# Kernel tuning notes

Measured on AMD Instinct MI355X. Metric: run time of the kernel, lower is better.

Reference implementation:

```python
import jax, jax.numpy as jnp
import numpy as np

N_OPS = 8  # eset_ops_3_to_3: identity, 3 single-axis sums, 3 pair sums, full sum (broadcast back)


def _conv(x, w, b):
    # x: (N,C,H,W), w: (O,C,kh,kw), VALID conv, stride 1
    y = jax.lax.conv_general_dilated(x, w, (1, 1), 'VALID',
                                     dimension_numbers=('NCHW', 'OIHW', 'NCHW'))
    return y + b[None, :, None, None]


def _maxpool2(x):
    return jax.lax.reduce_window(x, -jnp.inf, jax.lax.max,
                                 (1, 1, 2, 2), (1, 1, 2, 2), 'VALID')


def _eq3to3(x, W, b):
    # x: (B,i,j,k,d) channels-last; W: (N_OPS,d,o); b: (o,)
    # Fused form: contract each summed basis op with its weight BEFORE broadcasting.
    si = x.sum(1)          # (B,j,k,d)
    sj = x.sum(2)          # (B,i,k,d)
    sk = x.sum(3)          # (B,i,j,d)
    sij = x.sum((1, 2))    # (B,k,d)
    sik = x.sum((1, 3))    # (B,j,d)
    sjk = x.sum((2, 3))    # (B,i,d)
    s = x.sum((1, 2, 3))   # (B,d)
    y = jnp.einsum('bijkd,do->bijko', x, W[0])
    y = y + jnp.einsum('bjkd,do->bjko', si, W[1])[:, None]
    y = y + jnp.einsum('bikd,do->biko', sj, W[2])[:, :, None]
    y = y + jnp.einsum('bijd,do->bijo', sk, W[3])[:, :, :, None]
    y = y + jnp.einsum('bkd,do->bko', sij, W[4])[:, None, None]
    y = y + jnp.einsum('bjd,do->bjo', sik, W[5])[:, None, :, None]
    y = y + jnp.einsum('bid,do->bio', sjk, W[6])[:, :, None, None]
    y = y + jnp.einsum('bd,do->bo', s, W[7])[:, None, None, None]
    return y + b


def setup_inputs() -> dict:
    key = jax.random.key(0)
    ks = jax.random.split(key, 14)
    B, k, h, w = 16, 40, 28, 28
    hid, out_dim = 64, 32
    flat = 64 * 4 * 4  # after conv5-pool2-conv5-pool2 on 28x28
    p = lambda ki, shape, fan: jax.random.normal(ki, shape, jnp.float32) / np.sqrt(fan)
    return {
        'x': jax.random.normal(ks[0], (B, k, h, w), jnp.float32),
        'conv1_w': p(ks[1], (32, 1, 5, 5), 25),
        'conv1_b': jnp.zeros((32,), jnp.float32),
        'conv2_w': p(ks[2], (64, 32, 5, 5), 32 * 25),
        'conv2_b': jnp.zeros((64,), jnp.float32),
        'fc_w': p(ks[3], (flat, hid), flat),
        'fc_b': jnp.zeros((hid,), jnp.float32),
        'eq1_w': p(ks[4], (N_OPS, hid, hid), N_OPS * hid) * 0.1,
        'eq1_b': jnp.zeros((hid,), jnp.float32),
        'eq2_w': p(ks[5], (N_OPS, hid, out_dim), N_OPS * hid) * 0.1,
        'eq2_b': jnp.zeros((out_dim,), jnp.float32),
        'out_w': p(ks[6], (out_dim, 1), out_dim),
        'out_b': jnp.zeros((1,), jnp.float32),
    }


def reference(x, conv1_w, conv1_b, conv2_w, conv2_b, fc_w, fc_b,
              eq1_w, eq1_b, eq2_w, eq2_b, out_w, out_b):
    B, k, h, w = x.shape
    z = x.reshape(B * k, 1, h, w)
    z = _maxpool2(jax.nn.relu(_conv(z, conv1_w, conv1_b)))
    z = _maxpool2(jax.nn.relu(_conv(z, conv2_w, conv2_b)))
    z = z.reshape(B * k, -1) @ fc_w + fc_b
    e = jax.nn.relu(z).reshape(B, k, -1)          # (B,k,d)
    t = jnp.einsum('bid,bjd,bkd->bijkd', e, e, e)  # (B,k,k,k,d) cubic tensor
    y = jax.nn.relu(_eq3to3(t, eq1_w, eq1_b))
    y = _eq3to3(y, eq2_w, eq2_b)                   # (B,k,k,k,out_dim)
    y = jax.nn.relu(y).sum(axis=(1, 2, 3))         # (B,out_dim); dropout_prob=0 (eval)
    y = jax.nn.relu(y)
    return y @ out_w + out_b                       # (B,1)
```

## Files before the change

kernel.cpp:

```cpp
#include <hip/hip_runtime.h>
#include <hip/hip_bf16.h>


typedef unsigned short u16;
typedef __attribute__((ext_vector_type(8))) short bf8_t;
typedef __attribute__((ext_vector_type(4))) float f4_t;

#define LSTR 72

__device__ inline u16 f2bf(float f){
  union { float f; unsigned u; } v; v.f = f;
  unsigned r = v.u + 0x7fffu + ((v.u >> 16) & 1u);
  return (u16)(r >> 16);
}
__device__ inline float bflo(unsigned u){ union { unsigned x; float f; } v; v.x = u << 16; return v.f; }
__device__ inline float bfhi(unsigned u){ union { unsigned x; float f; } v; v.x = u & 0xffff0000u; return v.f; }
__device__ inline unsigned pack2(float a, float b){ return (unsigned)f2bf(a) | ((unsigned)f2bf(b) << 16); }
__device__ inline unsigned cvtpk(float lo, float hi){
  __hip_bfloat162 h2 = __float22bfloat162_rn(make_float2(lo, hi));
  union { __hip_bfloat162 h; unsigned u; } c; c.h = h2; return c.u;
}
__device__ inline void unpack8(bf8_t x, float* o){
  union { bf8_t v; unsigned u[4]; } q; q.v = x;
  #pragma unroll
  for (int p = 0; p < 4; ++p){ o[2*p] = bflo(q.u[p]); o[2*p+1] = bfhi(q.u[p]); }
}

__global__ __launch_bounds__(256) void kconv1(const float* __restrict__ x, const float* __restrict__ w1,
                                              const float* __restrict__ b1, u16* __restrict__ z1t,
                                              const float* __restrict__ w2, const float* __restrict__ fcw,
                                              u16* __restrict__ wt2, u16* __restrict__ fcwT){
  __shared__ float simg[784];
  int img = blockIdx.x, tid = threadIdx.x;
  if (img >= 640){
    int t = (img - 640)*256 + tid, stride = 32*256;
    for (int i = t; i < 51200; i += stride){
      int tap = i >> 11, rc = i & 2047, co = rc >> 5, ci = rc & 31;
      wt2[i] = f2bf(w2[co*800 + ci*25 + tap]);
    }
    for (int i = t; i < 65536; i += stride){
      int o = i >> 10, k = i & 1023;
      fcwT[i] = f2bf(fcw[k*64 + o]);
    }
    return;
  }
  for (int i = tid; i < 784; i += 256) simg[i] = x[img*784 + i];
  const int c = tid & 31;
  float wc[25];
  #pragma unroll
  for (int t = 0; t < 25; ++t) wc[t] = w1[c*25 + t];
  const float bb = b1[c];
  __syncthreads();
  #pragma unroll 2
  for (int it = 0; it < 18; ++it){
    int p = (tid >> 5) + it*8;
    int py = p / 12, px = p % 12;
    float patch[36];
    const float* sp = &simg[2*py*28 + 2*px];
    #pragma unroll
    for (int yy = 0; yy < 6; ++yy)
      #pragma unroll
      for (int xx = 0; xx < 6; ++xx) patch[yy*6+xx] = sp[yy*28+xx];
    float mx = -1e30f;
    #pragma unroll
    for (int sy = 0; sy < 2; ++sy)
    #pragma unroll
    for (int sx = 0; sx < 2; ++sx){
      float s = bb;
      #pragma unroll
      for (int dy = 0; dy < 5; ++dy)
        #pragma unroll
        for (int dx = 0; dx < 5; ++dx)
          s += patch[(sy+dy)*6 + sx+dx] * wc[dy*5+dx];
      mx = fmaxf(mx, s);
    }
    z1t[(size_t)img*4608 + p*32 + c] = f2bf(fmaxf(mx, 0.f));
  }
}

__global__ __launch_bounds__(256) void kconv2m(const u16* __restrict__ z1t, const u16* __restrict__ wt2,
                                               const float* __restrict__ b2, u16* __restrict__ z2g){
  __shared__ __align__(16) u16 sz[4608];
  __shared__ __align__(16) u16 sz2[1024];
  int img = blockIdx.x, tid = threadIdx.x;
  for (int i = tid; i < 576; i += 256)
    ((uint4*)sz)[i] = ((const uint4*)(z1t + (size_t)img*4608))[i];
  __syncthreads();
  const int wave = tid >> 6, lane = tid & 63, l15 = lane & 15, quad = lane >> 4;
  const int y = wave*2 + (l15 >> 3), x = l15 & 7;
  f4_t acc[4];
  acc[0] = (f4_t){0.f,0.f,0.f,0.f}; acc[1] = acc[0]; acc[2] = acc[0]; acc[3] = acc[0];
  #pragma unroll
  for (int dy = 0; dy < 5; ++dy)
    #pragma unroll
    for (int dx = 0; dx < 5; ++dx){
      const int tap = dy*5 + dx;
      bf8_t af = *(const bf8_t*)&sz[((y+dy)*12 + (x+dx))*32 + quad*8];
      const u16* wp = wt2 + tap*2048 + l15*32 + quad*8;
      #pragma unroll
      for (int nt = 0; nt < 4; ++nt){
        bf8_t bf = *(const bf8_t*)(wp + nt*512);
        acc[nt] = __builtin_amdgcn_mfma_f32_16x16x32_bf16(af, bf, acc[nt], 0, 0, 0);
      }
    }
  #pragma unroll
  for (int nt = 0; nt < 4; ++nt){
    int co = nt*16 + l15;
    float v0 = fmaxf(acc[nt][0], acc[nt][1]);
    float v1 = fmaxf(acc[nt][2], acc[nt][3]);
    v0 = fmaxf(v0, __shfl_xor(v0, 32));
    v1 = fmaxf(v1, __shfl_xor(v1, 32));
    if (quad < 2){
      float bb = b2[co];
      sz2[co*16 + wave*4 + quad*2 + 0] = f2bf(fmaxf(v0 + bb, 0.f));
      sz2[co*16 + wave*4 + quad*2 + 1] = f2bf(fmaxf(v1 + bb, 0.f));
    }
  }
  __syncthreads();
  if (tid < 128) ((uint4*)(z2g + (size_t)img*1024))[tid] = ((const uint4*)sz2)[tid];
}

__global__ __launch_bounds__(256) void kfc(const u16* __restrict__ z2g, const u16* __restrict__ fcwT,
                                           const float* __restrict__ fcb,
                                           float* __restrict__ e_f, u16* __restrict__ e_b){
  __shared__ __align__(16) u16 sA[16*1032];
  int img0 = blockIdx.x*16, tid = threadIdx.x;
  for (int i = tid; i < 2048; i += 256){
    int row = i >> 7, c16 = i & 127;
    ((uint4*)(sA + row*1032))[c16] = ((const uint4*)(z2g + (size_t)(img0+row)*1024))[c16];
  }
  __syncthreads();
  const int wave = tid >> 6, lane = tid & 63, l15 = lane & 15, quad = lane >> 4;
  const int o = wave*16 + l15;
  f4_t acc = (f4_t){0.f,0.f,0.f,0.f};
  #pragma unroll 8
  for (int ks = 0; ks < 32; ++ks){
    bf8_t af = *(const bf8_t*)&sA[l15*1032 + ks*32 + quad*8];
    bf8_t bf = *(const bf8_t*)(fcwT + (size_t)o*1024 + ks*32 + quad*8);
    acc = __builtin_amdgcn_mfma_f32_16x16x32_bf16(af, bf, acc, 0, 0, 0);
  }
  const float bb = fcb[o];
  #pragma unroll
  for (int r = 0; r < 4; ++r){
    int img = img0 + quad*4 + r;
    float v = fmaxf(acc[r] + bb, 0.f);
    e_f[img*64 + o] = v;
    e_b[img*64 + o] = f2bf(v);
  }
}

__global__ __launch_bounds__(256) void kprep(const float* __restrict__ e_f, const float* __restrict__ e1w,
    const float* __restrict__ e1b, const float* __restrict__ e2w,
    float* __restrict__ Sg, u16* __restrict__ Vt, float* __restrict__ c0,
    float* __restrict__ P5, float* __restrict__ P6, u16* __restrict__ W2T0,
    u16* __restrict__ W3St){
  int b = blockIdx.x, ph = blockIdx.y, tid = threadIdx.x;
  __shared__ float se[2560];
  __shared__ float S[64], S2[64], S3[64];
  for (int i = tid; i < 2560; i += 256) se[i] = e_f[b*2560 + i];
  __syncthreads();
  if (tid < 64){
    float s = 0.f;
    for (int i = 0; i < 40; ++i) s += se[i*64 + tid];
    S[tid] = s; S2[tid] = s*s; S3[tid] = s*s*s;
    if (ph == 0) Sg[b*64 + tid] = s;
  }
  __syncthreads();
  {
    const int m = ph;
    for (int idx = tid; idx < 4096; idx += 256){
      int o = idx >> 6, d = idx & 63;
      float v;
      if (m == 0)      v = e1w[d*64 + o];
      else if (m == 1) v = S[d] * e1w[4096  + d*64 + o];
      else if (m == 2) v = S[d] * e1w[8192  + d*64 + o];
      else             v = S2[d] * e1w[16384 + d*64 + o];
      Vt[(size_t)b*16384 + m*4096 + idx] = f2bf(v);
    }
  }
  if (ph == 0){
    if (tid < 64){
      float a = e1b[tid];
      for (int d = 0; d < 64; ++d) a += S3[d] * e1w[7*4096 + d*64 + tid];
      c0[b*64 + tid] = a;
    }
  } else if (ph == 1){
    for (int idx = tid; idx < 4096; idx += 256){
      int o = idx >> 6, d = idx & 63;
      W3St[(size_t)b*4096 + idx] = f2bf(S[d] * e1w[3*4096 + d*64 + o]);
    }
  } else {
    int lo = (ph == 2) ? 0 : 1280, hi = lo + 1280;
    for (int idx = lo + tid; idx < hi; idx += 256){
      int j = idx >> 6, o = idx & 63;
      float a5 = 0.f, a6 = 0.f;
      for (int d = 0; d < 64; ++d){
        float es = se[j*64 + d] * S2[d];
        a5 += es * e1w[5*4096 + d*64 + o];
        a6 += es * e1w[6*4096 + d*64 + o];
      }
      P5[(b*40+j)*64 + o] = a5;
      P6[(b*40+j)*64 + o] = a6;
    }
    if (ph == 3 && b == 0){
      for (int idx = tid; idx < 2048; idx += 256){
        int o = idx >> 6, d = idx & 63;
        W2T0[o*64 + d] = f2bf(e2w[d*32 + o]);
      }
    }
  }
}

__global__ __launch_bounds__(256) void kpq(const u16* __restrict__ e_b, const u16* __restrict__ W3St,
    const float* __restrict__ P5, const float* __restrict__ P6, const float* __restrict__ c0,
    float* __restrict__ Q3c){
  __shared__ __align__(16) u16 sP[48*LSTR];
  __shared__ __align__(16) u16 sW[64*LSTR];
  int blk = blockIdx.x, b = blk/40, i = blk%40, tid = threadIdx.x;
  const int wave = tid >> 6, lane = tid & 63, l15 = lane & 15, quad = lane >> 4;
  for (int idx = tid; idx < 2048; idx += 256){
    int o = idx >> 5, c = idx & 31;
    ((unsigned*)(sW + o*LSTR))[c] = ((const unsigned*)(W3St + (size_t)b*4096))[idx];
  }
  const unsigned* eb32 = (const unsigned*)(e_b + (size_t)b*2560);
  const unsigned* el = eb32 + i*32;
  #pragma unroll
  for (int it = 0; it < 6; ++it){
    int idx = tid + it*256;
    int k = idx >> 5, d2 = idx & 31;
    unsigned pv = 0;
    if (k < 40){
      unsigned ul = el[d2], uk = eb32[k*32 + d2];
      pv = pack2(bflo(ul)*bflo(uk), bfhi(ul)*bfhi(uk));
    }
    ((unsigned*)(sP + k*LSTR))[d2] = pv;
  }
  __syncthreads();
  bf8_t wf[2];
  #pragma unroll
  for (int ks = 0; ks < 2; ++ks)
    wf[ks] = *(const bf8_t*)&sW[(wave*16 + l15)*LSTR + ks*32 + quad*8];
  f4_t acc[3];
  #pragma unroll
  for (int n = 0; n < 3; ++n){
    f4_t a = (f4_t){0.f,0.f,0.f,0.f};
    #pragma unroll
    for (int ks = 0; ks < 2; ++ks){
      bf8_t pkf = *(const bf8_t*)&sP[(n*16 + l15)*LSTR + ks*32 + quad*8];
      a = __builtin_amdgcn_mfma_f32_16x16x32_bf16(wf[ks], pkf, a, 0, 0, 0);
    }
    acc[n] = a;
  }
  const int obase = wave*16 + quad*4;
  f4_t p6v = *(const f4_t*)&P6[(b*40+i)*64 + obase];
  f4_t c0v = *(const f4_t*)&c0[b*64 + obase];
  #pragma unroll
  for (int n = 0; n < 3; ++n){
    int j = n*16 + l15;
    if (j < 40){
      f4_t p5v = *(const f4_t*)&P5[(b*40+j)*64 + obase];
      f4_t outv = acc[n] + p5v + p6v + c0v;
      *(f4_t*)&Q3c[((size_t)((b*40+i)*40 + j))*64 + obase] = outv;
    }
  }
}

__global__ __launch_bounds__(256, 4) void kh01(
    const u16* __restrict__ e_b, const float* __restrict__ e_f,
    const u16* __restrict__ Vt, const float* __restrict__ Q3c,
    float* __restrict__ si2, float* __restrict__ sj2, float* __restrict__ sk2)
{
  __shared__ __align__(16) char smem[25344];
  u16*   sU  = (u16*)smem;
  u16*   sB1 = (u16*)(smem + 6912);
  u16*   sB0 = (u16*)(smem + 16128);
  float* sUf = (float*)smem;
  const int tid = threadIdx.x;
  const int b = blockIdx.x / 40, fix = blockIdx.x % 40;
  const int mode = blockIdx.y;
  const int wave = tid >> 6, lane = tid & 63, l15 = lane & 15, quad = lane >> 4;
  const f4_t z4 = (f4_t){0.f,0.f,0.f,0.f};

  for (int idx = tid; idx < 1536; idx += 256){
    int r = idx >> 5, c = idx & 31;
    unsigned v = (r < 40) ? ((const unsigned*)e_b)[(b*40 + r)*32 + c] : 0u;
    ((unsigned*)(sU + r*LSTR))[c] = v;
  }
  float efr[10];
  #pragma unroll
  for (int t = 0; t < 10; ++t) efr[t] = e_f[b*2560 + tid + t*256];
  const unsigned* eg = (const unsigned*)(e_b + (size_t)(b*40 + fix)*64);
  const unsigned* Vb = (const unsigned*)(Vt + (size_t)b*16384);
  for (int idx = tid; idx < 2048; idx += 256){
    int o = idx >> 5, d2 = idx & 31;
    unsigned eu = eg[d2];
    unsigned v0 = Vb[o*32 + d2];
    unsigned vA = Vb[(2-mode)*2048 + o*32 + d2];
    unsigned vB = Vb[(1+mode)*2048 + o*32 + d2];
    unsigned v3 = Vb[3*2048 + o*32 + d2];
    float e0 = bflo(eu), e1 = bfhi(eu);
    ((unsigned*)(sB1 + o*LSTR))[d2] = pack2(e0*bflo(v0)+bflo(vA), e1*bfhi(v0)+bfhi(vA));
    ((unsigned*)(sB0 + o*LSTR))[d2] = pack2(e0*bflo(vB)+bflo(v3), e1*bfhi(vB)+bfhi(v3));
  }
  __syncthreads();

  f4_t b1v[4];
  bf8_t ua[3][2];
  f4_t Y0[3];
  {
    bf8_t b0f[2], b1f[2];
    float tmp[8];
    #pragma unroll
    for (int ks = 0; ks < 2; ++ks){
      b1f[ks] = *(const bf8_t*)&sB1[(wave*16 + l15)*LSTR + ks*32 + quad*8];
      b0f[ks] = *(const bf8_t*)&sB0[(wave*16 + l15)*LSTR + ks*32 + quad*8];
      unpack8(b1f[ks], tmp);
      b1v[2*ks]   = (f4_t){tmp[0],tmp[1],tmp[2],tmp[3]};
      b1v[2*ks+1] = (f4_t){tmp[4],tmp[5],tmp[6],tmp[7]};
    }
    #pragma unroll
    for (int n = 0; n < 3; ++n){
      f4_t a = z4;
      #pragma unroll
      for (int ks = 0; ks < 2; ++ks){
        ua[n][ks] = *(const bf8_t*)&sU[(n*16 + l15)*LSTR + ks*32 + quad*8];
        a = __builtin_amdgcn_mfma_f32_16x16x32_bf16(b0f[ks], ua[n][ks], a, 0, 0, 0);
      }
      Y0[n] = a;
    }
  }
  __syncthreads();
  #pragma unroll
  for (int t = 0; t < 10; ++t) sUf[tid + t*256] = efr[t];
  __syncthreads();

  const int obase = wave*16 + quad*4;
  const float km = (l15 < 8) ? 1.f : 0.f;
  const f4_t km4 = (f4_t){km, km, km, km};
  f4_t sacc[3];
  sacc[0] = z4; sacc[1] = z4; sacc[2] = z4;

  auto qaddr = [&](int l) -> const f4_t* {
    int qidx = mode ? (fix*40 + l) : (l*40 + fix);
    return (const f4_t*)&Q3c[((size_t)(b*1600 + qidx))*64 + obase];
  };
  f4_t cadd_n = *qaddr(0);
  for (int l = 0; l < 40; ++l){
    f4_t cadd = cadd_n;
    if (l < 39) cadd_n = *qaddr(l + 1);
    const float* ep = &sUf[l*64 + quad*8];
    f4_t p00 = b1v[0] * *(const f4_t*)(ep);
    f4_t p01 = b1v[1] * *(const f4_t*)(ep + 4);
    f4_t p10 = b1v[2] * *(const f4_t*)(ep + 32);
    f4_t p11 = b1v[3] * *(const f4_t*)(ep + 36);
    union { bf8_t v; unsigned u[4]; } m0, m1;
    m0.u[0] = cvtpk(p00[0], p00[1]); m0.u[1] = cvtpk(p00[2], p00[3]);
    m0.u[2] = cvtpk(p01[0], p01[1]); m0.u[3] = cvtpk(p01[2], p01[3]);
    m1.u[0] = cvtpk(p10[0], p10[1]); m1.u[1] = cvtpk(p10[2], p10[3]);
    m1.u[2] = cvtpk(p11[0], p11[1]); m1.u[3] = cvtpk(p11[2], p11[3]);
    f4_t khs = z4;
    #pragma unroll
    for (int n = 0; n < 3; ++n){
      f4_t a = Y0[n];
      a = __builtin_amdgcn_mfma_f32_16x16x32_bf16(m0.v, ua[n][0], a, 0, 0, 0);
      a = __builtin_amdgcn_mfma_f32_16x16x32_bf16(m1.v, ua[n][1], a, 0, 0, 0);
      f4_t h = __builtin_elementwise_max(a + cadd, z4);
      sacc[n] += h;
      if (mode == 0) khs += (n == 2) ? h * km4 : h;
    }
    if (mode == 0){
      #pragma unroll
      for (int r = 0; r < 4; ++r){
        float v = khs[r];
        v += __shfl_xor(v, 1); v += __shfl_xor(v, 2);
        v += __shfl_xor(v, 4); v += __shfl_xor(v, 8);
        khs[r] = v;
      }
      if (l15 == 0)
        *(f4_t*)&sk2[((size_t)((b*40 + l)*40 + fix))*64 + obase] = khs;
    }
  }
  float* dst = mode ? sj2 : si2;
  #pragma unroll
  for (int n = 0; n < 3; ++n){
    int k = n*16 + l15;
    if (k < 40)
      *(f4_t*)&dst[((size_t)((b*40 + fix)*40 + k))*64 + obase] = sacc[n];
  }
}

__global__ __launch_bounds__(256) void k5a(const float* __restrict__ si2, const float* __restrict__ sj2,
    const float* __restrict__ e2w, const float* __restrict__ e2b,
    float* __restrict__ A4, float* __restrict__ A5, float* __restrict__ A6, float* __restrict__ A7){
  int b = blockIdx.x, half = blockIdx.y, tid = threadIdx.x;
  __shared__ float ssij[2560], ssik[2560], ssjk[2560], ss2[64];
  if (half == 0){
    for (int idx = tid; idx < 2560; idx += 256){
      int k = idx >> 6, d = idx & 63;
      float a = 0.f;
      for (int j = 0; j < 40; ++j) a += si2[((size_t)(b*40+j)*40 + k)*64 + d];
      ssij[idx] = a;
    }
  } else {
    for (int idx = tid; idx < 2560; idx += 256){
      int j = idx >> 6, d = idx & 63;
      float a = 0.f, c = 0.f;
      const float* p = &si2[(size_t)(b*40+j)*2560 + d];
      const float* q = &sj2[(size_t)(b*40+j)*2560 + d];
      for (int k = 0; k < 40; ++k){ a += p[k*64]; c += q[k*64]; }
      ssik[idx] = a;
      ssjk[idx] = c;
    }
  }
  __syncthreads();
  if (half == 0 && tid < 64){
    float a = 0.f;
    for (int k = 0; k < 40; ++k) a += ssij[k*64 + tid];
    ss2[tid] = a;
  }
  __syncthreads();
  if (half == 0){
    for (int idx = tid; idx < 1280; idx += 256){
      int k = idx >> 5, o = idx & 31;
      float a4 = 0.f;
      for (int d = 0; d < 64; ++d) a4 += ssij[k*64+d] * e2w[4*2048 + d*32 + o];
      A4[(b*40+k)*32 + o] = a4;
    }
    if (tid < 32){
      float a = e2b[tid];
      for (int d = 0; d < 64; ++d) a += ss2[d] * e2w[7*2048 + d*32 + tid];
      A7[b*32 + tid] = a;
    }
  } else {
    for (int idx = tid; idx < 1280; idx += 256){
      int k = idx >> 5, o = idx & 31;
      float a5 = 0.f, a6 = 0.f;
      for (int d = 0; d < 64; ++d){
        a5 += ssik[k*64+d] * e2w[5*2048 + d*32 + o];
        a6 += ssjk[k*64+d] * e2w[6*2048 + d*32 + o];
      }
      A5[(b*40+k)*32 + o] = a5;
      A6[(b*40+k)*32 + o] = a6;
    }
  }
}

__global__ __launch_bounds__(256) void k5b(const float* __restrict__ si2, const float* __restrict__ sj2,
    const float* __restrict__ sk2, const float* __restrict__ e2w,
    const float* __restrict__ A4, const float* __restrict__ A5, const float* __restrict__ A6,
    const float* __restrict__ A7,
    float* __restrict__ A1p, float* __restrict__ A2t, float* __restrict__ Cc){
  int which = blockIdx.y;
  int blk = blockIdx.x, b = blk/40, f = blk%40, tid = threadIdx.x;
  __shared__ __align__(16) f4_t ssrc[640];
  __shared__ __align__(16) f4_t swt[32*17];
  const float* S = (which == 0) ? si2 : (which == 1) ? sj2 : sk2;
  int wop = which + 1;
  const f4_t* Sg4 = (const f4_t*)&S[(size_t)(b*40+f)*2560];
  for (int idx = tid; idx < 640; idx += 256) ssrc[idx] = Sg4[idx];
  for (int idx = tid; idx < 512; idx += 256){
    int o = idx >> 4, d4 = idx & 15;
    f4_t w;
    #pragma unroll
    for (int r = 0; r < 4; ++r) w[r] = e2w[wop*2048 + (4*d4+r)*32 + o];
    swt[o*17 + d4] = w;
  }
  __syncthreads();
  const int o = tid & 31, rb = tid >> 5;
  float acc[5] = {0.f, 0.f, 0.f, 0.f, 0.f};
  #pragma unroll 4
  for (int d4 = 0; d4 < 16; ++d4){
    f4_t w = swt[o*17 + d4];
    #pragma unroll
    for (int it = 0; it < 5; ++it){
      f4_t s = ssrc[(rb + 8*it)*16 + d4];
      acc[it] += s[0]*w[0] + s[1]*w[1] + s[2]*w[2] + s[3]*w[3];
    }
  }
  #pragma unroll
  for (int it = 0; it < 5; ++it){
    int r = rb + 8*it;
    size_t oi = ((size_t)(b*40+f)*40 + r)*32 + o;
    float a = acc[it];
    if (which == 0)      A1p[oi] = a + A4[(b*40+r)*32 + o];
    else if (which == 1) A2t[oi] = a;
    else                 Cc[oi]  = a + A5[(b*40+r)*32 + o] + A6[(b*40+f)*32 + o] + A7[b*32 + o];
  }
}

__global__ __launch_bounds__(256, 3) void kh2(
    const u16* __restrict__ e_b, const float* __restrict__ e_f,
    const u16* __restrict__ Vt, const float* __restrict__ Q3c, const u16* __restrict__ W2T0,
    const float* __restrict__ A1p, const float* __restrict__ A2t, const float* __restrict__ Cc,
    float* __restrict__ out_part)
{
  __shared__ __align__(16) char smem[30080];
  u16*   sB1 = (u16*)smem;
  u16*   sB0 = (u16*)(smem + 9216);
  u16*   sU  = (u16*)(smem + 18432);
  u16*   sW2 = (u16*)(smem + 18432 + 6912);
  float* sUf = (float*)(smem + 18432);
  float* soacc = (float*)(smem + 29952);
  const int tid = threadIdx.x;
  const int b = blockIdx.x / 40, fix = blockIdx.x % 40;
  const int wave = tid >> 6, lane = tid & 63, l15 = lane & 15, quad = lane >> 4;
  const f4_t z4 = (f4_t){0.f,0.f,0.f,0.f};

  for (int idx = tid; idx < 1536; idx += 256){
    int r = idx >> 5, c = idx & 31;
    unsigned v = (r < 40) ? ((const unsigned*)e_b)[(b*40 + r)*32 + c] : 0u;
    ((unsigned*)(sU + r*LSTR))[c] = v;
  }
  float efr[10];
  #pragma unroll
  for (int t = 0; t < 10; ++t) efr[t] = e_f[b*2560 + tid + t*256];
  const unsigned* eg = (const unsigned*)(e_b + (size_t)(b*40 + fix)*64);
  const unsigned* Vb = (const unsigned*)(Vt + (size_t)b*16384);
  for (int idx = tid; idx < 2048; idx += 256){
    int o = idx >> 5, d2 = idx & 31;
    unsigned eu = eg[d2];
    unsigned v0 = Vb[o*32 + d2];
    unsigned vA = Vb[2*2048 + o*32 + d2];
    unsigned vB = Vb[1*2048 + o*32 + d2];
    unsigned v3 = Vb[3*2048 + o*32 + d2];
    float e0 = bflo(eu), e1 = bfhi(eu);
    ((unsigned*)(sB1 + o*LSTR))[d2] = pack2(e0*bflo(v0)+bflo(vA), e1*bfhi(v0)+bfhi(vA));
    ((unsigned*)(sB0 + o*LSTR))[d2] = pack2(e0*bflo(vB)+bflo(v3), e1*bfhi(vB)+bfhi(v3));
  }
  for (int idx = tid; idx < 1024; idx += 256){
    int o = idx >> 5, c = idx & 31;
    ((unsigned*)(sW2 + o*LSTR))[c] = ((const unsigned*)W2T0)[idx];
  }
  if (tid < 32) soacc[tid] = 0.f;
  __syncthreads();

  f4_t b1v[4];
  bf8_t ua[3][2], wfA[2][2];
  f4_t Y0[3];
  {
    bf8_t b0f[2], b1f[2];
    float tmp[8];
    #pragma unroll
    for (int ks = 0; ks < 2; ++ks){
      b1f[ks] = *(const bf8_t*)&sB1[(wave*16 + l15)*LSTR + ks*32 + quad*8];
      b0f[ks] = *(const bf8_t*)&sB0[(wave*16 + l15)*LSTR + ks*32 + quad*8];
      unpack8(b1f[ks], tmp);
      b1v[2*ks]   = (f4_t){tmp[0],tmp[1],tmp[2],tmp[3]};
      b1v[2*ks+1] = (f4_t){tmp[4],tmp[5],tmp[6],tmp[7]};
      #pragma unroll
      for (int m = 0; m < 2; ++m)
        wfA[m][ks] = *(const bf8_t*)&sW2[(m*16 + l15)*LSTR + ks*32 + quad*8];
    }
    #pragma unroll
    for (int n = 0; n < 3; ++n){
      f4_t a = z4;
      #pragma unroll
      for (int ks = 0; ks < 2; ++ks){
        ua[n][ks] = *(const bf8_t*)&sU[(n*16 + l15)*LSTR + ks*32 + quad*8];
        a = __builtin_amdgcn_mfma_f32_16x16x32_bf16(b0f[ks], ua[n][ks], a, 0, 0, 0);
      }
      Y0[n] = a;
    }
  }
  __syncthreads();
  #pragma unroll
  for (int t = 0; t < 10; ++t) sUf[tid + t*256] = efr[t];
  __syncthreads();

  const int obase = wave*16 + quad*4;
  const int o2b   = quad*4;
  const int kme   = wave*16 + l15;
  const int kmc   = kme < 40 ? kme : 39;
  const bool kval = (kme < 40) & (wave < 3);
  f4_t pa1[2], psum[2];
  psum[0] = z4; psum[1] = z4;
  if (wave < 3){
    #pragma unroll
    for (int m = 0; m < 2; ++m)
      pa1[m] = *(const f4_t*)&A1p[((size_t)((b*40 + fix)*40 + kmc))*32 + m*16 + o2b];
  }

  f4_t cadd_n = *(const f4_t*)&Q3c[((size_t)(b*1600 + 0*40 + fix))*64 + obase];
  for (int l = 0; l < 40; ++l){
    f4_t cadd = cadd_n;
    if (l < 39)
      cadd_n = *(const f4_t*)&Q3c[((size_t)(b*1600 + (l+1)*40 + fix))*64 + obase];
    f4_t a2v[2], ccv[2];
    if (wave < 3){
      #pragma unroll
      for (int m = 0; m < 2; ++m){
        a2v[m] = *(const f4_t*)&A2t[((size_t)((b*40 + l)*40 + kmc))*32 + m*16 + o2b];
        ccv[m] = *(const f4_t*)&Cc [((size_t)((b*40 + l)*40 + fix))*32 + m*16 + o2b];
      }
    }
    const float* ep = &sUf[l*64 + quad*8];
    f4_t p00 = b1v[0] * *(const f4_t*)(ep);
    f4_t p01 = b1v[1] * *(const f4_t*)(ep + 4);
    f4_t p10 = b1v[2] * *(const f4_t*)(ep + 32);
    f4_t p11 = b1v[3] * *(const f4_t*)(ep + 36);
    union { bf8_t v; unsigned u[4]; } m0, m1;
    m0.u[0] = cvtpk(p00[0], p00[1]); m0.u[1] = cvtpk(p00[2], p00[3]);
    m0.u[2] = cvtpk(p01[0], p01[1]); m0.u[3] = cvtpk(p01[2], p01[3]);
    m1.u[0] = cvtpk(p10[0], p10[1]); m1.u[1] = cvtpk(p10[2], p10[3]);
    m1.u[2] = cvtpk(p11[0], p11[1]); m1.u[3] = cvtpk(p11[2], p11[3]);
    u16* Hb = (u16*)(smem + (l & 1)*9216);
    #pragma unroll
    for (int n = 0; n < 3; ++n){
      f4_t a = Y0[n];
      a = __builtin_amdgcn_mfma_f32_16x16x32_bf16(m0.v, ua[n][0], a, 0, 0, 0);
      a = __builtin_amdgcn_mfma_f32_16x16x32_bf16(m1.v, ua[n][1], a, 0, 0, 0);
      f4_t h = __builtin_elementwise_max(a + cadd, z4);
      uint2 pw;
      pw.x = cvtpk(h[0], h[1]);
      pw.y = cvtpk(h[2], h[3]);
      *(uint2*)&Hb[(n*16 + l15)*LSTR + obase] = pw;
    }
    __syncthreads();
    if (wave < 3){
      bf8_t hB[2];
      #pragma unroll
      for (int ks = 0; ks < 2; ++ks)
        hB[ks] = *(const bf8_t*)&Hb[(wave*16 + l15)*LSTR + ks*32 + quad*8];
      #pragma unroll
      for (int m = 0; m < 2; ++m){
        f4_t y = z4;
        y = __builtin_amdgcn_mfma_f32_16x16x32_bf16(wfA[m][0], hB[0], y, 0, 0, 0);
        y = __builtin_amdgcn_mfma_f32_16x16x32_bf16(wfA[m][1], hB[1], y, 0, 0, 0);
        if (kval){
          f4_t v = y + pa1[m] + a2v[m] + ccv[m];
          psum[m] += __builtin_elementwise_max(v, z4);
        }
      }
    }
  }

  if (wave < 3){
    #pragma unroll
    for (int m = 0; m < 2; ++m)
      #pragma unroll
      for (int r = 0; r < 4; ++r){
        float v = psum[m][r];
        v += __shfl_xor(v, 1); v += __shfl_xor(v, 2);
        v += __shfl_xor(v, 4); v += __shfl_xor(v, 8);
        if (l15 == 0) atomicAdd(&soacc[m*16 + o2b + r], v);
      }
  }
  __syncthreads();
  if (tid < 32) out_part[(b*40 + fix)*32 + tid] = soacc[tid];
}

__global__ __launch_bounds__(512) void k7(const float* __restrict__ out_part, const float* __restrict__ ow,
                                          const float* __restrict__ ob, float* __restrict__ out){
  int tid = threadIdx.x;
  int b = tid >> 5, o = tid & 31;
  float s = 0.f;
  for (int j = 0; j < 40; ++j) s += out_part[(b*40 + j)*32 + o];
  s = s > 0.f ? s : 0.f;
  float v = s * ow[o];
  v += __shfl_xor(v, 1); v += __shfl_xor(v, 2); v += __shfl_xor(v, 4);
  v += __shfl_xor(v, 8); v += __shfl_xor(v, 16);
  if (o == 0) out[b] = v + ob[0];
}

extern "C" void kernel_launch(void* const* d_in, const int* in_sizes, int n_in,
                              void* d_out, int out_size, void* d_ws, size_t ws_size,
                              hipStream_t stream){
  const float* x    = (const float*)d_in[0];
  const float* c1w  = (const float*)d_in[1];
  const float* c1b  = (const float*)d_in[2];
  const float* c2w  = (const float*)d_in[3];
  const float* c2b  = (const float*)d_in[4];
  const float* fcw  = (const float*)d_in[5];
  const float* fcb  = (const float*)d_in[6];
  const float* e1w  = (const float*)d_in[7];
  const float* e1b  = (const float*)d_in[8];
  const float* e2w  = (const float*)d_in[9];
  const float* e2b  = (const float*)d_in[10];
  const float* ow   = (const float*)d_in[11];
  const float* ob   = (const float*)d_in[12];

  char* ws = (char*)d_ws;
  size_t off = 0;
  auto alloc = [&](size_t bytes) -> void* {
    void* p = ws + off;
    off += (bytes + 255) & ~(size_t)255;
    return p;
  };
  u16*   z1t  = (u16*)  alloc((size_t)640*4608*2);
  u16*   wt2  = (u16*)  alloc(51200*2);
  u16*   fcwT = (u16*)  alloc(65536*2);
  u16*   z2g  = (u16*)  alloc((size_t)640*1024*2);
  float* e_f  = (float*)alloc(40960*4);
  u16*   e_b  = (u16*)  alloc(40960*2);
  float* Sg   = (float*)alloc(1024*4);
  u16*   Vt   = (u16*)  alloc((size_t)16*16384*2);
  float* c0   = (float*)alloc(1024*4);
  float* P5   = (float*)alloc(40960*4);
  float* P6   = (float*)alloc(40960*4);
  u16*   W2T0 = (u16*)  alloc(2048*2);
  u16*   W3St = (u16*)  alloc((size_t)16*4096*2);
  float* Q3c  = (float*)alloc((size_t)1638400*4);
  float* si2  = (float*)alloc((size_t)1638400*4);
  float* sj2  = (float*)alloc((size_t)1638400*4);
  float* sk2  = (float*)alloc((size_t)1638400*4);
  float* A4   = (float*)alloc(20480*4);
  float* A5   = (float*)alloc(20480*4);
  float* A6   = (float*)alloc(20480*4);
  float* A7   = (float*)alloc(512*4);
  float* A1p  = (float*)alloc((size_t)819200*4);
  float* A2t  = (float*)alloc((size_t)819200*4);
  float* Cc   = (float*)alloc((size_t)819200*4);
  float* op   = (float*)alloc(20480*4);
  (void)in_sizes; (void)n_in; (void)out_size; (void)ws_size;

  kconv1 <<<672, 256, 0, stream>>>(x, c1w, c1b, z1t, c2w, fcw, wt2, fcwT);
  kconv2m<<<640, 256, 0, stream>>>(z1t, wt2, c2b, z2g);
  kfc    <<<40,  256, 0, stream>>>(z2g, fcwT, fcb, e_f, e_b);
  kprep  <<<dim3(16,4), 256, 0, stream>>>(e_f, e1w, e1b, e2w, Sg, Vt, c0, P5, P6, W2T0, W3St);
  kpq    <<<640, 256, 0, stream>>>(e_b, W3St, P5, P6, c0, Q3c);
  kh01   <<<dim3(640,2), 256, 0, stream>>>(e_b, e_f, Vt, Q3c, si2, sj2, sk2);
  k5a    <<<dim3(16,2), 256, 0, stream>>>(si2, sj2, e2w, e2b, A4, A5, A6, A7);
  k5b    <<<dim3(640,3), 256, 0, stream>>>(si2, sj2, sk2, e2w, A4, A5, A6, A7, A1p, A2t, Cc);
  kh2    <<<640, 256, 0, stream>>>(e_b, e_f, Vt, Q3c, W2T0, A1p, A2t, Cc, op);
  k7     <<<1, 512, 0, stream>>>(op, ow, ob, (float*)d_out);
}
```

Baseline: 293.2 us.

## Split k5a reductions into wider-parallel kernel and strength-reduce inner loop addressing

The k5a reduction stage ran on only 32 blocks. It is split into k5ar, which computes the pair-sum reductions over a 16x3x2 grid and writes them to global scratch, and k5am, which loads those sums and applies the weight matmuls. The inner loops of kh01 and kh2 switch from per-iteration index arithmetic to incrementing pointers, are unrolled by 2, and use vector-wide xor shuffles for the lane reductions. This adds one kernel launch and an extra global round-trip for the reduced sums.

```diff
diff --git a/kernel.cpp b/kernel.cpp
--- a/kernel.cpp
+++ b/kernel.cpp
@@ -24,6 +24,12 @@
   union { bf8_t v; unsigned u[4]; } q; q.v = x;
   #pragma unroll
   for (int p = 0; p < 4; ++p){ o[2*p] = bflo(q.u[p]); o[2*p+1] = bfhi(q.u[p]); }
+}
+__device__ inline f4_t shfl4x(f4_t v, int m){
+  f4_t r;
+  r[0] = __shfl_xor(v[0], m); r[1] = __shfl_xor(v[1], m);
+  r[2] = __shfl_xor(v[2], m); r[3] = __shfl_xor(v[3], m);
+  return r;
 }
 
 __global__ __launch_bounds__(256) void kconv1(const float* __restrict__ x, const float* __restrict__ w1,
@@ -340,19 +346,21 @@
   f4_t sacc[3];
   sacc[0] = z4; sacc[1] = z4; sacc[2] = z4;
 
-  auto qaddr = [&](int l) -> const f4_t* {
-    int qidx = mode ? (fix*40 + l) : (l*40 + fix);
-    return (const f4_t*)&Q3c[((size_t)(b*1600 + qidx))*64 + obase];
-  };
-  f4_t cadd_n = *qaddr(0);
+  const int qstride = mode ? 64 : 2560;
+  const float* qp = Q3c + (size_t)b*102400 + (mode ? (size_t)fix*2560 : (size_t)fix*64) + obase;
+  float* skp = sk2 + ((size_t)(b*40)*40 + fix)*64 + obase;
+  const float* ep = sUf + quad*8;
+
+  f4_t cadd_n = *(const f4_t*)qp; qp += qstride;
+  #pragma unroll 2
   for (int l = 0; l < 40; ++l){
     f4_t cadd = cadd_n;
-    if (l < 39) cadd_n = *qaddr(l + 1);
-    const float* ep = &sUf[l*64 + quad*8];
+    if (l < 39){ cadd_n = *(const f4_t*)qp; qp += qstride; }
     f4_t p00 = b1v[0] * *(const f4_t*)(ep);
     f4_t p01 = b1v[1] * *(const f4_t*)(ep + 4);
     f4_t p10 = b1v[2] * *(const f4_t*)(ep + 32);
     f4_t p11 = b1v[3] * *(const f4_t*)(ep + 36);
+    ep += 64;
     union { bf8_t v; unsigned u[4]; } m0, m1;
     m0.u[0] = cvtpk(p00[0], p00[1]); m0.u[1] = cvtpk(p00[2], p00[3]);
     m0.u[2] = cvtpk(p01[0], p01[1]); m0.u[3] = cvtpk(p01[2], p01[3]);
@@ -369,15 +377,12 @@
       if (mode == 0) khs += (n == 2) ? h * km4 : h;
     }
     if (mode == 0){
-      #pragma unroll
-      for (int r = 0; r < 4; ++r){
-        float v = khs[r];
-        v += __shfl_xor(v, 1); v += __shfl_xor(v, 2);
-        v += __shfl_xor(v, 4); v += __shfl_xor(v, 8);
-        khs[r] = v;
-      }
-      if (l15 == 0)
-        *(f4_t*)&sk2[((size_t)((b*40 + l)*40 + fix))*64 + obase] = khs;
+      khs += shfl4x(khs, 1);
+      khs += shfl4x(khs, 2);
+      khs += shfl4x(khs, 4);
+      khs += shfl4x(khs, 8);
+      if (l15 == 0) *(f4_t*)skp = khs;
+      skp += 2560;
     }
   }
   float* dst = mode ? sj2 : si2;
@@ -389,41 +394,46 @@
   }
 }
 
-__global__ __launch_bounds__(256) void k5a(const float* __restrict__ si2, const float* __restrict__ sj2,
-    const float* __restrict__ e2w, const float* __restrict__ e2b,
+__global__ __launch_bounds__(256) void k5ar(const float* __restrict__ si2, const float* __restrict__ sj2,
+    float* __restrict__ ssij, float* __restrict__ ssik, float* __restrict__ ssjk){
+  int b = blockIdx.x, which = blockIdx.y, half = blockIdx.z, tid = threadIdx.x;
+  int base = half*1280;
+  for (int idx = base + tid; idx < base + 1280; idx += 256){
+    int r = idx >> 6, d = idx & 63;
+    float a = 0.f;
+    if (which == 0){
+      for (int j = 0; j < 40; ++j) a += si2[((size_t)(b*40+j)*40 + r)*64 + d];
+      ssij[b*2560 + idx] = a;
+    } else if (which == 1){
+      const float* p = &si2[(size_t)(b*40+r)*2560 + d];
+      for (int k = 0; k < 40; ++k) a += p[k*64];
+      ssik[b*2560 + idx] = a;
+    } else {
+      const float* q = &sj2[(size_t)(b*40+r)*2560 + d];
+      for (int k = 0; k < 40; ++k) a += q[k*64];
+      ssjk[b*2560 + idx] = a;
+    }
+  }
+}
+
+__global__ __launch_bounds__(256) void k5am(const float* __restrict__ ssij, const float* __restrict__ ssik,
+    const float* __restrict__ ssjk, const float* __restrict__ e2w, const float* __restrict__ e2b,
     float* __restrict__ A4, float* __restrict__ A5, float* __restrict__ A6, float* __restrict__ A7){
   int b = blockIdx.x, half = blockIdx.y, tid = threadIdx.x;
-  __shared__ float ssij[2560], ssik[2560], ssjk[2560], ss2[64];
+  __shared__ float s1[2560], s2[2560], ss2[64];
   if (half == 0){
-    for (int idx = tid; idx < 2560; idx += 256){
-      int k = idx >> 6, d = idx & 63;
+    for (int i = tid; i < 2560; i += 256) s1[i] = ssij[b*2560 + i];
+    __syncthreads();
+    if (tid < 64){
       float a = 0.f;
-      for (int j = 0; j < 40; ++j) a += si2[((size_t)(b*40+j)*40 + k)*64 + d];
-      ssij[idx] = a;
-    }
-  } else {
-    for (int idx = tid; idx < 2560; idx += 256){
-      int j = idx >> 6, d = idx & 63;
-      float a = 0.f, c = 0.f;
-      const float* p = &si2[(size_t)(b*40+j)*2560 + d];
-      const float* q = &sj2[(size_t)(b*40+j)*2560 + d];
-      for (int k = 0; k < 40; ++k){ a += p[k*64]; c += q[k*64]; }
-      ssik[idx] = a;
-      ssjk[idx] = c;
-    }
-  }
-  __syncthreads();
-  if (half == 0 && tid < 64){
-    float a = 0.f;
-    for (int k = 0; k < 40; ++k) a += ssij[k*64 + tid];
-    ss2[tid] = a;
-  }
-  __syncthreads();
-  if (half == 0){
+      for (int k = 0; k < 40; ++k) a += s1[k*64 + tid];
+      ss2[tid] = a;
+    }
+    __syncthreads();
     for (int idx = tid; idx < 1280; idx += 256){
       int k = idx >> 5, o = idx & 31;
       float a4 = 0.f;
-      for (int d = 0; d < 64; ++d) a4 += ssij[k*64+d] * e2w[4*2048 + d*32 + o];
+      for (int d = 0; d < 64; ++d) a4 += s1[k*64+d] * e2w[4*2048 + d*32 + o];
       A4[(b*40+k)*32 + o] = a4;
     }
     if (tid < 32){
@@ -432,12 +442,14 @@
       A7[b*32 + tid] = a;
     }
   } else {
+    for (int i = tid; i < 2560; i += 256){ s1[i] = ssik[b*2560 + i]; s2[i] = ssjk[b*2560 + i]; }
+    __syncthreads();
     for (int idx = tid; idx < 1280; idx += 256){
       int k = idx >> 5, o = idx & 31;
       float a5 = 0.f, a6 = 0.f;
       for (int d = 0; d < 64; ++d){
-        a5 += ssik[k*64+d] * e2w[5*2048 + d*32 + o];
-        a6 += ssjk[k*64+d] * e2w[6*2048 + d*32 + o];
+        a5 += s1[k*64+d] * e2w[5*2048 + d*32 + o];
+        a6 += s2[k*64+d] * e2w[6*2048 + d*32 + o];
       }
       A5[(b*40+k)*32 + o] = a5;
       A6[(b*40+k)*32 + o] = a6;
@@ -580,24 +592,27 @@
       pa1[m] = *(const f4_t*)&A1p[((size_t)((b*40 + fix)*40 + kmc))*32 + m*16 + o2b];
   }
 
-  f4_t cadd_n = *(const f4_t*)&Q3c[((size_t)(b*1600 + 0*40 + fix))*64 + obase];
+  const float* qp  = Q3c + (size_t)b*102400 + (size_t)fix*64 + obase;
+  const float* a2p = A2t + ((size_t)b*1600 + kmc)*32 + o2b;
+  const float* ccp = Cc  + ((size_t)b*1600 + fix)*32 + o2b;
+  const float* ep  = sUf + quad*8;
+
+  f4_t cadd_n = *(const f4_t*)qp; qp += 2560;
+  #pragma unroll 2
   for (int l = 0; l < 40; ++l){
     f4_t cadd = cadd_n;
-    if (l < 39)
-      cadd_n = *(const f4_t*)&Q3c[((size_t)(b*1600 + (l+1)*40 + fix))*64 + obase];
+    if (l < 39){ cadd_n = *(const f4_t*)qp; qp += 2560; }
     f4_t a2v[2], ccv[2];
     if (wave < 3){
-      #pragma unroll
-      for (int m = 0; m < 2; ++m){
-        a2v[m] = *(const f4_t*)&A2t[((size_t)((b*40 + l)*40 + kmc))*32 + m*16 + o2b];
-        ccv[m] = *(const f4_t*)&Cc [((size_t)((b*40 + l)*40 + fix))*32 + m*16 + o2b];
-      }
-    }
-    const float* ep = &sUf[l*64 + quad*8];
+      a2v[0] = *(const f4_t*)(a2p);      a2v[1] = *(const f4_t*)(a2p + 16);
+      ccv[0] = *(const f4_t*)(ccp);      ccv[1] = *(const f4_t*)(ccp + 16);
+    }
+    a2p += 1280; ccp += 1280;
     f4_t p00 = b1v[0] * *(const f4_t*)(ep);
     f4_t p01 = b1v[1] * *(const f4_t*)(ep + 4);
     f4_t p10 = b1v[2] * *(const f4_t*)(ep + 32);
     f4_t p11 = b1v[3] * *(const f4_t*)(ep + 36);
+    ep += 64;
     union { bf8_t v; unsigned u[4]; } m0, m1;
     m0.u[0] = cvtpk(p00[0], p00[1]); m0.u[1] = cvtpk(p00[2], p00[3]);
     m0.u[2] = cvtpk(p01[0], p01[1]); m0.u[3] = cvtpk(p01[2], p01[3]);
@@ -636,14 +651,14 @@
 
   if (wave < 3){
     #pragma unroll
-    for (int m = 0; m < 2; ++m)
-      #pragma unroll
-      for (int r = 0; r < 4; ++r){
-        float v = psum[m][r];
-        v += __shfl_xor(v, 1); v += __shfl_xor(v, 2);
-        v += __shfl_xor(v, 4); v += __shfl_xor(v, 8);
-        if (l15 == 0) atomicAdd(&soacc[m*16 + o2b + r], v);
+    for (int m = 0; m < 2; ++m){
+      f4_t v = psum[m];
+      v += shfl4x(v, 1); v += shfl4x(v, 2); v += shfl4x(v, 4); v += shfl4x(v, 8);
+      if (l15 == 0){
+        #pragma unroll
+        for (int r = 0; r < 4; ++r) atomicAdd(&soacc[m*16 + o2b + r], v[r]);
       }
+    }
   }
   __syncthreads();
   if (tid < 32) out_part[(b*40 + fix)*32 + tid] = soacc[tid];
@@ -703,6 +718,9 @@
   float* si2  = (float*)alloc((size_t)1638400*4);
   float* sj2  = (float*)alloc((size_t)1638400*4);
   float* sk2  = (float*)alloc((size_t)1638400*4);
+  float* ssij = (float*)alloc(40960*4);
+  float* ssik = (float*)alloc(40960*4);
+  float* ssjk = (float*)alloc(40960*4);
   float* A4   = (float*)alloc(20480*4);
   float* A5   = (float*)alloc(20480*4);
   float* A6   = (float*)alloc(20480*4);
@@ -719,7 +737,8 @@
   kprep  <<<dim3(16,4), 256, 0, stream>>>(e_f, e1w, e1b, e2w, Sg, Vt, c0, P5, P6, W2T0, W3St);
   kpq    <<<640, 256, 0, stream>>>(e_b, W3St, P5, P6, c0, Q3c);
   kh01   <<<dim3(640,2), 256, 0, stream>>>(e_b, e_f, Vt, Q3c, si2, sj2, sk2);
-  k5a    <<<dim3(16,2), 256, 0, stream>>>(si2, sj2, e2w, e2b, A4, A5, A6, A7);
+  k5ar   <<<dim3(16,3,2), 256, 0, stream>>>(si2, sj2, ssij, ssik, ssjk);
+  k5am   <<<dim3(16,2), 256, 0, stream>>>(ssij, ssik, ssjk, e2w, e2b, A4, A5, A6, A7);
   k5b    <<<dim3(640,3), 256, 0, stream>>>(si2, sj2, sk2, e2w, A4, A5, A6, A7, A1p, A2t, Cc);
   kh2    <<<640, 256, 0, stream>>>(e_b, e_f, Vt, Q3c, W2T0, A1p, A2t, Cc, op);
   k7     <<<1, 512, 0, stream>>>(op, ow, ob, (float*)d_out);
```

After: 279.1 us (median of 2 runs). 1.05x faster.
